# Performance work log

Measured on AMD Instinct MI355X. Metric: run time of the kernel, lower is better.

The kernel has to match this reference:

```python
import jax, jax.numpy as jnp
import numpy as np

NEG_SLOPE = 0.2  # PyG GATConv default leaky_relu slope
EPS = 1e-16      # PyG softmax denominator epsilon


def gat_conv(x, src, dst, n_nodes, W, att_src, att_dst, bias, concat):
    # x: [N, Din]; W: [Din, H*F]; att_src/att_dst: [H, F]; bias: [H*F] or [F]
    H, F = att_src.shape
    h = (x @ W).reshape(n_nodes, H, F)                 # [N, H, F]
    a_src = jnp.einsum('nhf,hf->nh', h, att_src)       # [N, H]
    a_dst = jnp.einsum('nhf,hf->nh', h, att_dst)       # [N, H]
    e = jax.nn.leaky_relu(a_src[src] + a_dst[dst], NEG_SLOPE)  # [E, H]
    # segment softmax over incoming edges of each destination node
    m = jax.ops.segment_max(e, dst, num_segments=n_nodes)      # [N, H]
    ex = jnp.exp(e - m[dst])                                   # [E, H]
    s = jax.ops.segment_sum(ex, dst, num_segments=n_nodes)     # [N, H]
    alpha = ex / (s[dst] + EPS)                                # [E, H]
    msg = alpha[:, :, None] * h[src]                           # [E, H, F]
    out = jax.ops.segment_sum(msg, dst, num_segments=n_nodes)  # [N, H, F]
    if concat:
        out = out.reshape(n_nodes, H * F)
    else:
        out = out.mean(axis=1)
    return out + bias


def setup_inputs() -> dict:
    key = jax.random.key(0)
    ks = jax.random.split(key, 12)
    N, E, Din, Fh, H, C = 50000, 800000, 512, 32, 8, 40
    x = jax.random.normal(ks[0], (N, Din), dtype=jnp.float32)
    edge_index = jax.random.randint(ks[1], (2, E), 0, N, dtype=jnp.int64)
    g1 = 1.0 / np.sqrt(Din)
    g2 = 1.0 / np.sqrt(H * Fh)
    return {
        'x': x,
        'edge_index': edge_index,
        'W1': jax.random.normal(ks[2], (Din, H * Fh), dtype=jnp.float32) * g1,
        'att_src1': jax.random.normal(ks[3], (H, Fh), dtype=jnp.float32) * g2,
        'att_dst1': jax.random.normal(ks[4], (H, Fh), dtype=jnp.float32) * g2,
        'b1': jnp.zeros((H * Fh,), dtype=jnp.float32),
        'W2': jax.random.normal(ks[5], (H * Fh, C), dtype=jnp.float32) * g2,
        'att_src2': jax.random.normal(ks[6], (1, C), dtype=jnp.float32) * 0.1,
        'att_dst2': jax.random.normal(ks[7], (1, C), dtype=jnp.float32) * 0.1,
        'b2': jnp.zeros((C,), dtype=jnp.float32),
    }


def reference(x, edge_index, W1, att_src1, att_dst1, b1, W2, att_src2, att_dst2, b2):
    N = x.shape[0]
    # PyG GATConv adds self-loops by default
    loop = jnp.arange(N, dtype=edge_index.dtype)
    src = jnp.concatenate([edge_index[0], loop])
    dst = jnp.concatenate([edge_index[1], loop])
    # eval mode: dropout layers are identity
    h = gat_conv(x, src, dst, N, W1, att_src1, att_dst1, b1, concat=True)
    h = jax.nn.elu(h)
    out = gat_conv(h, src, dst, N, W2, att_src2, att_dst2, b2, concat=False)
    return jax.nn.log_softmax(out, axis=1)
```

## Files before the change

### kernel.cpp

```cpp
#include <hip/hip_runtime.h>
#include <hip/hip_bf16.h>
#include <math.h>

#define NN_DIN 512
#define NN_HF  256
#define NN_H   8
#define NN_F   32
#define NN_C   40

typedef short bf16x8 __attribute__((ext_vector_type(8)));
typedef float f32x4 __attribute__((ext_vector_type(4)));

__device__ __forceinline__ unsigned short f2bf_rne(float x) {
    unsigned u = __builtin_bit_cast(unsigned, x);
    unsigned r = u + 0x7FFFu + ((u >> 16) & 1u);
    return (unsigned short)(r >> 16);
}
__device__ __forceinline__ float bfu2f(unsigned short s) {
    unsigned u = ((unsigned)s) << 16;
    return __builtin_bit_cast(float, u);
}

__global__ __launch_bounds__(256) void w1rne_kernel(
    const float* __restrict__ W1, unsigned short* __restrict__ Wh)
{
    __shared__ float tile[32][33];
    int bk = blockIdx.x * 32;
    int bn = blockIdx.y * 32;
    int tx = threadIdx.x & 31, ty = threadIdx.x >> 5;
    #pragma unroll
    for (int i = 0; i < 32; i += 8)
        tile[ty + i][tx] = W1[(size_t)(bk + ty + i) * NN_HF + bn + tx];
    __syncthreads();
    #pragma unroll
    for (int i = 0; i < 32; i += 8) {
        float v = tile[tx][ty + i];
        Wh[(size_t)(bn + ty + i) * NN_DIN + bk + tx] = f2bf_rne(v);
    }
}

#define G1_BM 64
#define G1_BN 256
#define G1_BK 64
#define G1_LDK 72

__global__ __launch_bounds__(256) void gemm1_kernel(
    const float* __restrict__ A, const unsigned short* __restrict__ BT,
    unsigned short* __restrict__ Cb, int M)
{
    __shared__ unsigned short Ah[G1_BM][G1_LDK];
    __shared__ unsigned short Bh[G1_BN][G1_LDK];
    const int m0 = blockIdx.x * G1_BM;
    const int tid = threadIdx.x;
    const int wave = tid >> 6, lane = tid & 63;
    const int wn = wave;
    const int lr = lane & 15, lg = lane >> 4;

    const int amr[4] = { (tid + 0*256) >> 4, (tid + 1*256) >> 4,
                         (tid + 2*256) >> 4, (tid + 3*256) >> 4 };
    const int akc = (tid & 15) << 2;
    const int bnr[8] = { (tid + 0*256) >> 3, (tid + 1*256) >> 3,
                         (tid + 2*256) >> 3, (tid + 3*256) >> 3,
                         (tid + 4*256) >> 3, (tid + 5*256) >> 3,
                         (tid + 6*256) >> 3, (tid + 7*256) >> 3 };
    const int bkc = (tid & 7) << 3;

    f32x4 acc[4][4];
    #pragma unroll
    for (int i = 0; i < 4; ++i)
        #pragma unroll
        for (int j = 0; j < 4; ++j) acc[i][j] = (f32x4){0.f, 0.f, 0.f, 0.f};

    float4 ra[4];
    bf16x8 rb[8];

    #pragma unroll
    for (int i = 0; i < 4; ++i) {
        ra[i] = make_float4(0.f, 0.f, 0.f, 0.f);
        if (m0 + amr[i] < M)
            ra[i] = *(const float4*)(A + (size_t)(m0 + amr[i]) * NN_DIN + akc);
    }
    #pragma unroll
    for (int i = 0; i < 8; ++i)
        rb[i] = *(const bf16x8*)(BT + (size_t)bnr[i] * NN_DIN + bkc);
    #pragma unroll
    for (int i = 0; i < 4; ++i) {
        ushort4 hv;
        hv.x = f2bf_rne(ra[i].x); hv.y = f2bf_rne(ra[i].y);
        hv.z = f2bf_rne(ra[i].z); hv.w = f2bf_rne(ra[i].w);
        *reinterpret_cast<ushort4*>(&Ah[amr[i]][akc]) = hv;
    }
    #pragma unroll
    for (int i = 0; i < 8; ++i)
        *reinterpret_cast<bf16x8*>(&Bh[bnr[i]][bkc]) = rb[i];
    __syncthreads();

    const int NSTEP = NN_DIN / G1_BK;
    for (int step = 0; step < NSTEP; ++step) {
        const bool last = (step == NSTEP - 1);
        if (!last) {
            int k0 = (step + 1) * G1_BK;
            #pragma unroll
            for (int i = 0; i < 4; ++i) {
                ra[i] = make_float4(0.f, 0.f, 0.f, 0.f);
                if (m0 + amr[i] < M)
                    ra[i] = *(const float4*)(A + (size_t)(m0 + amr[i]) * NN_DIN + k0 + akc);
            }
            #pragma unroll
            for (int i = 0; i < 8; ++i)
                rb[i] = *(const bf16x8*)(BT + (size_t)bnr[i] * NN_DIN + k0 + bkc);
        }
        #pragma unroll
        for (int ks = 0; ks < 2; ++ks) {
            const int kb = (ks << 5) + (lg << 3);
            bf16x8 fah[4], fbh[4];
            #pragma unroll
            for (int mi = 0; mi < 4; ++mi) {
                int m = (mi << 4) + lr;
                fah[mi] = *reinterpret_cast<const bf16x8*>(&Ah[m][kb]);
            }
            #pragma unroll
            for (int ni = 0; ni < 4; ++ni) {
                int n = (wn << 6) + (ni << 4) + lr;
                fbh[ni] = *reinterpret_cast<const bf16x8*>(&Bh[n][kb]);
            }
            #pragma unroll
            for (int mi = 0; mi < 4; ++mi)
                #pragma unroll
                for (int ni = 0; ni < 4; ++ni)
                    acc[mi][ni] = __builtin_amdgcn_mfma_f32_16x16x32_bf16(
                        fah[mi], fbh[ni], acc[mi][ni], 0, 0, 0);
        }
        __syncthreads();
        if (!last) {
            #pragma unroll
            for (int i = 0; i < 4; ++i) {
                ushort4 hv;
                hv.x = f2bf_rne(ra[i].x); hv.y = f2bf_rne(ra[i].y);
                hv.z = f2bf_rne(ra[i].z); hv.w = f2bf_rne(ra[i].w);
                *reinterpret_cast<ushort4*>(&Ah[amr[i]][akc]) = hv;
            }
            #pragma unroll
            for (int i = 0; i < 8; ++i)
                *reinterpret_cast<bf16x8*>(&Bh[bnr[i]][bkc]) = rb[i];
            __syncthreads();
        }
    }
    #pragma unroll
    for (int mi = 0; mi < 4; ++mi)
        #pragma unroll
        for (int ni = 0; ni < 4; ++ni)
            #pragma unroll
            for (int r = 0; r < 4; ++r) {
                int row = m0 + (mi << 4) + (lg << 2) + r;
                int col = (wn << 6) + (ni << 4) + lr;
                if (row < M)
                    Cb[(size_t)row * NN_HF + col] = f2bf_rne(acc[mi][ni][r]);
            }
}

__global__ __launch_bounds__(256) void attn1_kernel(
    const unsigned short* __restrict__ h1b, const float* __restrict__ att_s,
    const float* __restrict__ att_d, float* __restrict__ a1s,
    float* __restrict__ a1d)
{
    int n = blockIdx.x;
    int t = threadIdx.x;
    float hv = bfu2f(h1b[(size_t)n * NN_HF + t]);
    float ps = hv * att_s[t];
    float pd = hv * att_d[t];
    #pragma unroll
    for (int off = 16; off >= 1; off >>= 1) {
        ps += __shfl_down(ps, off, 32);
        pd += __shfl_down(pd, off, 32);
    }
    if ((t & 31) == 0) {
        a1s[n * NN_H + (t >> 5)] = ps;
        a1d[n * NN_H + (t >> 5)] = pd;
    }
}

__global__ void count_kernel(const int* __restrict__ dst, int* __restrict__ deg,
                             int E, int Nn)
{
    int e = blockIdx.x * blockDim.x + threadIdx.x;
    int Et = E + Nn;
    if (e >= Et) return;
    int d = (e < E) ? dst[e] : (e - E);
    atomicAdd(&deg[d], 1);
}

#define SCAN_CHUNK 1024
__global__ __launch_bounds__(256) void scan1_kernel(
    const int* __restrict__ deg, int* __restrict__ offs,
    int* __restrict__ bsums, int Nn)
{
    __shared__ int sh[256];
    int b = blockIdx.x, t = threadIdx.x;
    int base = b * SCAN_CHUNK + t * 4;
    int v[4];
    int tot = 0;
    #pragma unroll
    for (int i = 0; i < 4; ++i) {
        v[i] = (base + i < Nn) ? deg[base + i] : 0;
        tot += v[i];
    }
    sh[t] = tot;
    __syncthreads();
    for (int off = 1; off < 256; off <<= 1) {
        int y = (t >= off) ? sh[t - off] : 0;
        __syncthreads();
        sh[t] += y;
        __syncthreads();
    }
    int p = sh[t] - tot;
    #pragma unroll
    for (int i = 0; i < 4; ++i) {
        if (base + i < Nn) offs[base + i] = p;
        p += v[i];
    }
    if (t == 255) bsums[b] = sh[255];
}

__global__ void scan2_kernel(int* __restrict__ bsums, int nb)
{
    if (threadIdx.x == 0) {
        int run = 0;
        for (int i = 0; i < nb; ++i) {
            int tmp = bsums[i];
            bsums[i] = run;
            run += tmp;
        }
    }
}

__global__ void scan3_kernel(int* __restrict__ offs, const int* __restrict__ bsums,
                             int Nn, int Et)
{
    int i = blockIdx.x * blockDim.x + threadIdx.x;
    if (i < Nn) offs[i] += bsums[i >> 10];
    if (i == 0) offs[Nn] = Et;
}

__global__ void fill_kernel(const int* __restrict__ src, const int* __restrict__ dst,
                            const int* __restrict__ offs, int* __restrict__ cursor,
                            int* __restrict__ srcs, int E, int Nn)
{
    int e = blockIdx.x * blockDim.x + threadIdx.x;
    int Et = E + Nn;
    if (e >= Et) return;
    int d, s;
    if (e < E) { d = dst[e]; s = src[e]; }
    else       { d = e - E;  s = e - E;  }
    int pos = offs[d] + atomicAdd(&cursor[d], 1);
    srcs[pos] = s;
}

__global__ __launch_bounds__(256) void attw1_kernel(
    const float* __restrict__ a1s, const float* __restrict__ a1d,
    const int* __restrict__ offs, const int* __restrict__ srcs,
    float* __restrict__ alpha1, int Nn)
{
    int n = blockIdx.x * 4 + (threadIdx.x >> 6);
    if (n >= Nn) return;
    int lane = threadIdx.x & 63;
    int g = lane >> 3, h = lane & 7;
    int beg = offs[n], end = offs[n + 1];
    float adn = a1d[n * NN_H + h];
    float m = -3.0e38f, s = 0.f;
    for (int k = beg + g; k < end; k += 8) {
        int sN = srcs[k];
        float e = a1s[sN * NN_H + h] + adn;
        e = e > 0.f ? e : 0.2f * e;
        float nm = fmaxf(m, e);
        float sc = __expf(m - nm);
        s = s * sc + __expf(e - nm);
        m = nm;
    }
    #pragma unroll
    for (int off = 8; off < 64; off <<= 1) {
        float mo = __shfl_xor(m, off);
        float so = __shfl_xor(s, off);
        float nm = fmaxf(m, mo);
        s = s * __expf(m - nm) + so * __expf(mo - nm);
        m = nm;
    }
    float inv = 1.f / (s + 1e-16f);
    for (int k = beg + g; k < end; k += 8) {
        int sN = srcs[k];
        float e = a1s[sN * NN_H + h] + adn;
        e = e > 0.f ? e : 0.2f * e;
        alpha1[(size_t)k * NN_H + h] = __expf(e - m) * inv;
    }
}

__global__ __launch_bounds__(256) void agg1_kernel(
    const unsigned short* __restrict__ h1b, const float* __restrict__ alpha1,
    const int* __restrict__ offs, const int* __restrict__ srcs,
    const float* __restrict__ b1, unsigned short* __restrict__ hp1b, int Nn)
{
    int n = blockIdx.x * 4 + (threadIdx.x >> 6);
    if (n >= Nn) return;
    int lane = threadIdx.x & 63;
    int h = lane >> 3;
    int beg = offs[n], end = offs[n + 1];
    f32x4 a0 = {0.f,0.f,0.f,0.f}, a1 = a0, a2 = a0, a3 = a0;
    int k = beg;
    for (; k + 3 < end; k += 4) {
        int s0 = srcs[k], s1 = srcs[k+1], s2 = srcs[k+2], s3 = srcs[k+3];
        float w0 = alpha1[(size_t)k * NN_H + h];
        float w1 = alpha1[(size_t)(k+1) * NN_H + h];
        float w2 = alpha1[(size_t)(k+2) * NN_H + h];
        float w3 = alpha1[(size_t)(k+3) * NN_H + h];
        ushort4 v0 = *(const ushort4*)(h1b + (size_t)s0 * NN_HF + lane * 4);
        ushort4 v1 = *(const ushort4*)(h1b + (size_t)s1 * NN_HF + lane * 4);
        ushort4 v2 = *(const ushort4*)(h1b + (size_t)s2 * NN_HF + lane * 4);
        ushort4 v3 = *(const ushort4*)(h1b + (size_t)s3 * NN_HF + lane * 4);
        a0.x = fmaf(w0, bfu2f(v0.x), a0.x); a0.y = fmaf(w0, bfu2f(v0.y), a0.y);
        a0.z = fmaf(w0, bfu2f(v0.z), a0.z); a0.w = fmaf(w0, bfu2f(v0.w), a0.w);
        a1.x = fmaf(w1, bfu2f(v1.x), a1.x); a1.y = fmaf(w1, bfu2f(v1.y), a1.y);
        a1.z = fmaf(w1, bfu2f(v1.z), a1.z); a1.w = fmaf(w1, bfu2f(v1.w), a1.w);
        a2.x = fmaf(w2, bfu2f(v2.x), a2.x); a2.y = fmaf(w2, bfu2f(v2.y), a2.y);
        a2.z = fmaf(w2, bfu2f(v2.z), a2.z); a2.w = fmaf(w2, bfu2f(v2.w), a2.w);
        a3.x = fmaf(w3, bfu2f(v3.x), a3.x); a3.y = fmaf(w3, bfu2f(v3.y), a3.y);
        a3.z = fmaf(w3, bfu2f(v3.z), a3.z); a3.w = fmaf(w3, bfu2f(v3.w), a3.w);
    }
    for (; k < end; ++k) {
        int s0 = srcs[k];
        float w0 = alpha1[(size_t)k * NN_H + h];
        ushort4 v0 = *(const ushort4*)(h1b + (size_t)s0 * NN_HF + lane * 4);
        a0.x = fmaf(w0, bfu2f(v0.x), a0.x); a0.y = fmaf(w0, bfu2f(v0.y), a0.y);
        a0.z = fmaf(w0, bfu2f(v0.z), a0.z); a0.w = fmaf(w0, bfu2f(v0.w), a0.w);
    }
    f32x4 acc;
    acc[0] = (a0.x + a1.x) + (a2.x + a3.x);
    acc[1] = (a0.y + a1.y) + (a2.y + a3.y);
    acc[2] = (a0.z + a1.z) + (a2.z + a3.z);
    acc[3] = (a0.w + a1.w) + (a2.w + a3.w);
    float4 bb = *(const float4*)(b1 + lane * 4);
    float r0 = acc[0] + bb.x, r1 = acc[1] + bb.y;
    float r2 = acc[2] + bb.z, r3 = acc[3] + bb.w;
    r0 = r0 > 0.f ? r0 : __expf(r0) - 1.f;
    r1 = r1 > 0.f ? r1 : __expf(r1) - 1.f;
    r2 = r2 > 0.f ? r2 : __expf(r2) - 1.f;
    r3 = r3 > 0.f ? r3 : __expf(r3) - 1.f;
    ushort4 o = make_ushort4(f2bf_rne(r0), f2bf_rne(r1), f2bf_rne(r2), f2bf_rne(r3));
    *(ushort4*)(hp1b + (size_t)n * NN_HF + lane * 4) = o;
}

#define G2_ROWS 64
#define G2_KC   64

__global__ __launch_bounds__(256) void gemm2_kernel(
    const unsigned short* __restrict__ Ab, const float* __restrict__ W2,
    const float* __restrict__ att_s, const float* __restrict__ att_d,
    float* __restrict__ h2, float* __restrict__ a2s, float* __restrict__ a2d,
    int M)
{
    __shared__ float As[G2_ROWS][G2_KC + 1];
    __shared__ float Ws[G2_KC][NN_C];
    int m0 = blockIdx.x * G2_ROWS;
    int t = threadIdx.x;
    int rp = t >> 3;
    int cg = t & 7;
    int c0 = cg * 5;
    int r0 = rp * 2, r1 = r0 + 1;
    float acc[2][5] = {};
    for (int kc = 0; kc < NN_HF; kc += G2_KC) {
        #pragma unroll
        for (int i = 0; i < 4; ++i) {
            int g = t + i * 256;
            int r = g >> 4;
            int k4 = (g & 15) << 2;
            ushort4 v = make_ushort4(0, 0, 0, 0);
            if (m0 + r < M)
                v = *(const ushort4*)(Ab + (size_t)(m0 + r) * NN_HF + kc + k4);
            As[r][k4 + 0] = bfu2f(v.x); As[r][k4 + 1] = bfu2f(v.y);
            As[r][k4 + 2] = bfu2f(v.z); As[r][k4 + 3] = bfu2f(v.w);
        }
        #pragma unroll
        for (int i = 0; i < 10; ++i) {
            int g = t + i * 256;
            int k = g / NN_C, c = g % NN_C;
            Ws[k][c] = W2[(size_t)(kc + k) * NN_C + c];
        }
        __syncthreads();
        #pragma unroll 4
        for (int k = 0; k < G2_KC; ++k) {
            float a0 = As[r0][k];
            float a1 = As[r1][k];
            #pragma unroll
            for (int j = 0; j < 5; ++j) {
                float w = Ws[k][c0 + j];
                acc[0][j] += a0 * w;
                acc[1][j] += a1 * w;
            }
        }
        __syncthreads();
    }
    #pragma unroll
    for (int i = 0; i < 2; ++i) {
        int m = m0 + r0 + i;
        float ps = 0.f, pd = 0.f;
        #pragma unroll
        for (int j = 0; j < 5; ++j) {
            float v = acc[i][j];
            ps += v * att_s[c0 + j];
            pd += v * att_d[c0 + j];
            if (m < M) h2[(size_t)m * NN_C + c0 + j] = v;
        }
        #pragma unroll
        for (int off = 4; off >= 1; off >>= 1) {
            ps += __shfl_down(ps, off, 8);
            pd += __shfl_down(pd, off, 8);
        }
        if (cg == 0 && m < M) { a2s[m] = ps; a2d[m] = pd; }
    }
}

__global__ __launch_bounds__(256) void attw2_kernel(
    const float* __restrict__ a2s, const float* __restrict__ a2d,
    const int* __restrict__ offs, const int* __restrict__ srcs,
    float* __restrict__ alpha2, int Nn)
{
    int n = blockIdx.x * 4 + (threadIdx.x >> 6);
    if (n >= Nn) return;
    int lane = threadIdx.x & 63;
    int beg = offs[n], end = offs[n + 1];
    float adn = a2d[n];
    float m = -3.0e38f, s = 0.f;
    for (int k = beg + lane; k < end; k += 64) {
        int sN = srcs[k];
        float e = a2s[sN] + adn;
        e = e > 0.f ? e : 0.2f * e;
        float nm = fmaxf(m, e);
        float sc = __expf(m - nm);
        s = s * sc + __expf(e - nm);
        m = nm;
    }
    #pragma unroll
    for (int off = 1; off < 64; off <<= 1) {
        float mo = __shfl_xor(m, off);
        float so = __shfl_xor(s, off);
        float nm = fmaxf(m, mo);
        s = s * __expf(m - nm) + so * __expf(mo - nm);
        m = nm;
    }
    float inv = 1.f / (s + 1e-16f);
    for (int k = beg + lane; k < end; k += 64) {
        int sN = srcs[k];
        float e = a2s[sN] + adn;
        e = e > 0.f ? e : 0.2f * e;
        alpha2[k] = __expf(e - m) * inv;
    }
}

__global__ __launch_bounds__(256) void agg2_kernel(
    const float* __restrict__ h2, const float* __restrict__ alpha2,
    const int* __restrict__ offs, const int* __restrict__ srcs,
    const float* __restrict__ b2, float* __restrict__ out, int Nn)
{
    int n = blockIdx.x * 4 + (threadIdx.x >> 6);
    if (n >= Nn) return;
    int f = threadIdx.x & 63;
    int beg = offs[n], end = offs[n + 1];
    float a0 = 0.f, a1 = 0.f, a2 = 0.f, a3 = 0.f;
    int k = beg;
    for (; k + 3 < end; k += 4) {
        int s0 = srcs[k], s1 = srcs[k+1], s2 = srcs[k+2], s3 = srcs[k+3];
        float w0 = alpha2[k], w1 = alpha2[k+1], w2 = alpha2[k+2], w3 = alpha2[k+3];
        float h0 = (f < NN_C) ? h2[(size_t)s0 * NN_C + f] : 0.f;
        float h1 = (f < NN_C) ? h2[(size_t)s1 * NN_C + f] : 0.f;
        float h2v = (f < NN_C) ? h2[(size_t)s2 * NN_C + f] : 0.f;
        float h3 = (f < NN_C) ? h2[(size_t)s3 * NN_C + f] : 0.f;
        a0 = fmaf(w0, h0, a0); a1 = fmaf(w1, h1, a1);
        a2 = fmaf(w2, h2v, a2); a3 = fmaf(w3, h3, a3);
    }
    for (; k < end; ++k) {
        int s0 = srcs[k];
        float w0 = alpha2[k];
        float h0 = (f < NN_C) ? h2[(size_t)s0 * NN_C + f] : 0.f;
        a0 = fmaf(w0, h0, a0);
    }
    float acc = (a0 + a1) + (a2 + a3);
    float v = acc + ((f < NN_C) ? b2[f] : 0.f);
    float lg = (f < NN_C) ? v : -INFINITY;
    float mx = lg;
    #pragma unroll
    for (int off = 32; off >= 1; off >>= 1) mx = fmaxf(mx, __shfl_xor(mx, off));
    float w2e = (f < NN_C) ? __expf(lg - mx) : 0.f;
    float sum = w2e;
    #pragma unroll
    for (int off = 32; off >= 1; off >>= 1) sum += __shfl_xor(sum, off);
    if (f < NN_C) out[(size_t)n * NN_C + f] = lg - mx - __logf(sum);
}

extern "C" void kernel_launch(void* const* d_in, const int* in_sizes, int n_in,
                              void* d_out, int out_size, void* d_ws, size_t ws_size,
                              hipStream_t stream)
{
    const float* x    = (const float*)d_in[0];
    const int*   ei   = (const int*)d_in[1];
    const float* W1   = (const float*)d_in[2];
    const float* as1  = (const float*)d_in[3];
    const float* ad1  = (const float*)d_in[4];
    const float* b1   = (const float*)d_in[5];
    const float* W2   = (const float*)d_in[6];
    const float* as2  = (const float*)d_in[7];
    const float* ad2  = (const float*)d_in[8];
    const float* b2   = (const float*)d_in[9];
    float* out = (float*)d_out;

    int Nn = in_sizes[0] / NN_DIN;
    int E  = in_sizes[1] / 2;
    int Et = E + Nn;
    const int* srcIdx = ei;
    const int* dstIdx = ei + E;

    char* ws = (char*)d_ws;
    size_t off = 0;
    auto alloc = [&](size_t bytes) {
        void* p = ws + off;
        off = (off + bytes + 255) & ~(size_t)255;
        return p;
    };
    unsigned short* h1b  = (unsigned short*)alloc((size_t)Nn * NN_HF * 2);
    unsigned short* W1T  = (unsigned short*)alloc((size_t)NN_HF * NN_DIN * 2);
    unsigned short* hp1b = (unsigned short*)alloc((size_t)Nn * NN_HF * 2);
    float* a1s  = (float*)alloc((size_t)Nn * NN_H * 4);
    float* a1d  = (float*)alloc((size_t)Nn * NN_H * 4);
    float* h2   = (float*)alloc((size_t)Nn * NN_C * 4);
    float* a2s  = (float*)alloc((size_t)Nn * 4);
    float* a2d  = (float*)alloc((size_t)Nn * 4);
    float* alpha1 = (float*)alloc((size_t)Et * NN_H * 4);
    float* alpha2 = (float*)alloc((size_t)Et * 4);
    int*   deg  = (int*)alloc((size_t)Nn * 4);
    int*   offs = (int*)alloc((size_t)(Nn + 1) * 4);
    int*   bsums= (int*)alloc(1024 * 4);
    int*   curs = (int*)alloc((size_t)Nn * 4);
    int*   srcs = (int*)alloc((size_t)Et * 4);

    hipMemsetAsync(deg, 0, (size_t)Nn * 4, stream);
    hipMemsetAsync(curs, 0, (size_t)Nn * 4, stream);

    w1rne_kernel<<<dim3(NN_DIN / 32, NN_HF / 32), 256, 0, stream>>>(W1, W1T);

    gemm1_kernel<<<(Nn + G1_BM - 1) / G1_BM, 256, 0, stream>>>(x, W1T, h1b, Nn);

    attn1_kernel<<<Nn, 256, 0, stream>>>(h1b, as1, ad1, a1s, a1d);

    count_kernel<<<(Et + 255) / 256, 256, 0, stream>>>(dstIdx, deg, E, Nn);
    int nb = (Nn + SCAN_CHUNK - 1) / SCAN_CHUNK;
    scan1_kernel<<<nb, 256, 0, stream>>>(deg, offs, bsums, Nn);
    scan2_kernel<<<1, 64, 0, stream>>>(bsums, nb);
    scan3_kernel<<<(Nn + 255) / 256, 256, 0, stream>>>(offs, bsums, Nn, Et);
    fill_kernel<<<(Et + 255) / 256, 256, 0, stream>>>(srcIdx, dstIdx, offs, curs, srcs, E, Nn);

    attw1_kernel<<<(Nn + 3) / 4, 256, 0, stream>>>(a1s, a1d, offs, srcs, alpha1, Nn);
    agg1_kernel<<<(Nn + 3) / 4, 256, 0, stream>>>(h1b, alpha1, offs, srcs, b1, hp1b, Nn);

    gemm2_kernel<<<(Nn + G2_ROWS - 1) / G2_ROWS, 256, 0, stream>>>(
        hp1b, W2, as2, ad2, h2, a2s, a2d, Nn);

    attw2_kernel<<<(Nn + 3) / 4, 256, 0, stream>>>(a2s, a2d, offs, srcs, alpha2, Nn);
    agg2_kernel<<<(Nn + 3) / 4, 256, 0, stream>>>(h2, alpha2, offs, srcs, b2, out, Nn);
}
```

Measured before the change: 494.3 us.

## Fuse attention softmax into aggregation kernels and move gemm2 to bf16 MFMA

Merges attw1 into agg1 and attw2 into agg2. The softmax max and sum are now computed inside the aggregation kernel, and edge weights are recomputed on the fly instead of being written to and read back from alpha buffers. This removes two launches and the per-edge alpha traffic, at the cost of re-gathering a1s/a2s per edge. Separately, gemm2 is rewritten to use bf16 16x16x32 MFMA with a transposed, bf16-rounded W2 (padded to 48 columns) produced by a new small conversion kernel. The padding adds some wasted MFMA work, and W2 now passes through bf16 rounding.

```diff
diff --git a/kernel.cpp b/kernel.cpp
--- a/kernel.cpp
+++ b/kernel.cpp
@@ -37,6 +37,18 @@
         float v = tile[tx][ty + i];
         Wh[(size_t)(bn + ty + i) * NN_DIN + bk + tx] = f2bf_rne(v);
     }
+}
+
+__global__ __launch_bounds__(256) void w2rne_kernel(
+    const float* __restrict__ W2, unsigned short* __restrict__ W2T)
+{
+    int idx = blockIdx.x * 256 + threadIdx.x;
+    if (idx >= 48 * 256) return;
+    int c = idx >> 8;
+    int k = idx & 255;
+    unsigned short v = 0;
+    if (c < NN_C) v = f2bf_rne(W2[(size_t)k * NN_C + c]);
+    W2T[idx] = v;
 }
 
 #define G1_BM 64
@@ -256,25 +268,25 @@
     srcs[pos] = s;
 }
 
-__global__ __launch_bounds__(256) void attw1_kernel(
-    const float* __restrict__ a1s, const float* __restrict__ a1d,
-    const int* __restrict__ offs, const int* __restrict__ srcs,
-    float* __restrict__ alpha1, int Nn)
+__global__ __launch_bounds__(256) void agg1_kernel(
+    const unsigned short* __restrict__ h1b, const float* __restrict__ a1s,
+    const float* __restrict__ a1d, const int* __restrict__ offs,
+    const int* __restrict__ srcs, const float* __restrict__ b1,
+    unsigned short* __restrict__ hp1b, int Nn)
 {
     int n = blockIdx.x * 4 + (threadIdx.x >> 6);
     if (n >= Nn) return;
     int lane = threadIdx.x & 63;
-    int g = lane >> 3, h = lane & 7;
     int beg = offs[n], end = offs[n + 1];
-    float adn = a1d[n * NN_H + h];
+
+    int g = lane >> 3, hh = lane & 7;
+    float adn1 = a1d[n * NN_H + hh];
     float m = -3.0e38f, s = 0.f;
     for (int k = beg + g; k < end; k += 8) {
-        int sN = srcs[k];
-        float e = a1s[sN * NN_H + h] + adn;
+        float e = a1s[srcs[k] * NN_H + hh] + adn1;
         e = e > 0.f ? e : 0.2f * e;
         float nm = fmaxf(m, e);
-        float sc = __expf(m - nm);
-        s = s * sc + __expf(e - nm);
+        s = s * __expf(m - nm) + __expf(e - nm);
         m = nm;
     }
     #pragma unroll
@@ -286,32 +298,26 @@
         m = nm;
     }
     float inv = 1.f / (s + 1e-16f);
-    for (int k = beg + g; k < end; k += 8) {
-        int sN = srcs[k];
-        float e = a1s[sN * NN_H + h] + adn;
-        e = e > 0.f ? e : 0.2f * e;
-        alpha1[(size_t)k * NN_H + h] = __expf(e - m) * inv;
-    }
-}
-
-__global__ __launch_bounds__(256) void agg1_kernel(
-    const unsigned short* __restrict__ h1b, const float* __restrict__ alpha1,
-    const int* __restrict__ offs, const int* __restrict__ srcs,
-    const float* __restrict__ b1, unsigned short* __restrict__ hp1b, int Nn)
-{
-    int n = blockIdx.x * 4 + (threadIdx.x >> 6);
-    if (n >= Nn) return;
-    int lane = threadIdx.x & 63;
+
     int h = lane >> 3;
-    int beg = offs[n], end = offs[n + 1];
+    float mh   = __shfl(m, h);
+    float invh = __shfl(inv, h);
+    float adn  = __shfl(adn1, h);
+
     f32x4 a0 = {0.f,0.f,0.f,0.f}, a1 = a0, a2 = a0, a3 = a0;
     int k = beg;
     for (; k + 3 < end; k += 4) {
         int s0 = srcs[k], s1 = srcs[k+1], s2 = srcs[k+2], s3 = srcs[k+3];
-        float w0 = alpha1[(size_t)k * NN_H + h];
-        float w1 = alpha1[(size_t)(k+1) * NN_H + h];
-        float w2 = alpha1[(size_t)(k+2) * NN_H + h];
-        float w3 = alpha1[(size_t)(k+3) * NN_H + h];
+        float e0 = a1s[s0 * NN_H + h] + adn;
+        float e1 = a1s[s1 * NN_H + h] + adn;
+        float e2 = a1s[s2 * NN_H + h] + adn;
+        float e3 = a1s[s3 * NN_H + h] + adn;
+        e0 = e0 > 0.f ? e0 : 0.2f * e0;  e1 = e1 > 0.f ? e1 : 0.2f * e1;
+        e2 = e2 > 0.f ? e2 : 0.2f * e2;  e3 = e3 > 0.f ? e3 : 0.2f * e3;
+        float w0 = __expf(e0 - mh) * invh;
+        float w1 = __expf(e1 - mh) * invh;
+        float w2 = __expf(e2 - mh) * invh;
+        float w3 = __expf(e3 - mh) * invh;
         ushort4 v0 = *(const ushort4*)(h1b + (size_t)s0 * NN_HF + lane * 4);
         ushort4 v1 = *(const ushort4*)(h1b + (size_t)s1 * NN_HF + lane * 4);
         ushort4 v2 = *(const ushort4*)(h1b + (size_t)s2 * NN_HF + lane * 4);
@@ -327,7 +333,9 @@
     }
     for (; k < end; ++k) {
         int s0 = srcs[k];
-        float w0 = alpha1[(size_t)k * NN_H + h];
+        float e0 = a1s[s0 * NN_H + h] + adn;
+        e0 = e0 > 0.f ? e0 : 0.2f * e0;
+        float w0 = __expf(e0 - mh) * invh;
         ushort4 v0 = *(const ushort4*)(h1b + (size_t)s0 * NN_HF + lane * 4);
         a0.x = fmaf(w0, bfu2f(v0.x), a0.x); a0.y = fmaf(w0, bfu2f(v0.y), a0.y);
         a0.z = fmaf(w0, bfu2f(v0.z), a0.z); a0.w = fmaf(w0, bfu2f(v0.w), a0.w);
@@ -348,94 +356,132 @@
     *(ushort4*)(hp1b + (size_t)n * NN_HF + lane * 4) = o;
 }
 
-#define G2_ROWS 64
-#define G2_KC   64
+#define G2_BM 128
 
 __global__ __launch_bounds__(256) void gemm2_kernel(
-    const unsigned short* __restrict__ Ab, const float* __restrict__ W2,
+    const unsigned short* __restrict__ Ab, const unsigned short* __restrict__ W2T,
     const float* __restrict__ att_s, const float* __restrict__ att_d,
     float* __restrict__ h2, float* __restrict__ a2s, float* __restrict__ a2d,
     int M)
 {
-    __shared__ float As[G2_ROWS][G2_KC + 1];
-    __shared__ float Ws[G2_KC][NN_C];
-    int m0 = blockIdx.x * G2_ROWS;
-    int t = threadIdx.x;
-    int rp = t >> 3;
-    int cg = t & 7;
-    int c0 = cg * 5;
-    int r0 = rp * 2, r1 = r0 + 1;
-    float acc[2][5] = {};
-    for (int kc = 0; kc < NN_HF; kc += G2_KC) {
+    __shared__ unsigned short Ah[G2_BM][72];
+    __shared__ unsigned short Bh[48][72];
+    const int m0 = blockIdx.x * G2_BM;
+    const int tid = threadIdx.x;
+    const int wave = tid >> 6, lane = tid & 63;
+    const int lr = lane & 15, lg = lane >> 4;
+
+    f32x4 acc[2][3];
+    #pragma unroll
+    for (int i = 0; i < 2; ++i)
+        #pragma unroll
+        for (int j = 0; j < 3; ++j) acc[i][j] = (f32x4){0.f, 0.f, 0.f, 0.f};
+
+    for (int kc = 0; kc < NN_HF; kc += 64) {
         #pragma unroll
         for (int i = 0; i < 4; ++i) {
-            int g = t + i * 256;
-            int r = g >> 4;
-            int k4 = (g & 15) << 2;
-            ushort4 v = make_ushort4(0, 0, 0, 0);
+            int gi = tid + i * 256;
+            int r = gi >> 3;
+            int k8 = (gi & 7) << 3;
+            bf16x8 v = (bf16x8){0,0,0,0,0,0,0,0};
             if (m0 + r < M)
-                v = *(const ushort4*)(Ab + (size_t)(m0 + r) * NN_HF + kc + k4);
-            As[r][k4 + 0] = bfu2f(v.x); As[r][k4 + 1] = bfu2f(v.y);
-            As[r][k4 + 2] = bfu2f(v.z); As[r][k4 + 3] = bfu2f(v.w);
-        }
-        #pragma unroll
-        for (int i = 0; i < 10; ++i) {
-            int g = t + i * 256;
-            int k = g / NN_C, c = g % NN_C;
-            Ws[k][c] = W2[(size_t)(kc + k) * NN_C + c];
+                v = *(const bf16x8*)(Ab + (size_t)(m0 + r) * NN_HF + kc + k8);
+            *reinterpret_cast<bf16x8*>(&Ah[r][k8]) = v;
+        }
+        #pragma unroll
+        for (int i = 0; i < 2; ++i) {
+            int gi = tid + i * 256;
+            if (gi < 384) {
+                int r = gi >> 3;
+                int k8 = (gi & 7) << 3;
+                *reinterpret_cast<bf16x8*>(&Bh[r][k8]) =
+                    *(const bf16x8*)(W2T + (size_t)r * NN_HF + kc + k8);
+            }
         }
         __syncthreads();
-        #pragma unroll 4
-        for (int k = 0; k < G2_KC; ++k) {
-            float a0 = As[r0][k];
-            float a1 = As[r1][k];
-            #pragma unroll
-            for (int j = 0; j < 5; ++j) {
-                float w = Ws[k][c0 + j];
-                acc[0][j] += a0 * w;
-                acc[1][j] += a1 * w;
-            }
+        #pragma unroll
+        for (int ks = 0; ks < 2; ++ks) {
+            const int kb = (ks << 5) + (lg << 3);
+            bf16x8 fa[2], fb[3];
+            #pragma unroll
+            for (int mi = 0; mi < 2; ++mi) {
+                int r = (wave << 5) + (mi << 4) + lr;
+                fa[mi] = *reinterpret_cast<const bf16x8*>(&Ah[r][kb]);
+            }
+            #pragma unroll
+            for (int ni = 0; ni < 3; ++ni) {
+                int c = (ni << 4) + lr;
+                fb[ni] = *reinterpret_cast<const bf16x8*>(&Bh[c][kb]);
+            }
+            #pragma unroll
+            for (int mi = 0; mi < 2; ++mi)
+                #pragma unroll
+                for (int ni = 0; ni < 3; ++ni)
+                    acc[mi][ni] = __builtin_amdgcn_mfma_f32_16x16x32_bf16(
+                        fa[mi], fb[ni], acc[mi][ni], 0, 0, 0);
         }
         __syncthreads();
     }
-    #pragma unroll
-    for (int i = 0; i < 2; ++i) {
-        int m = m0 + r0 + i;
-        float ps = 0.f, pd = 0.f;
-        #pragma unroll
-        for (int j = 0; j < 5; ++j) {
-            float v = acc[i][j];
-            ps += v * att_s[c0 + j];
-            pd += v * att_d[c0 + j];
-            if (m < M) h2[(size_t)m * NN_C + c0 + j] = v;
-        }
-        #pragma unroll
-        for (int off = 4; off >= 1; off >>= 1) {
-            ps += __shfl_down(ps, off, 8);
-            pd += __shfl_down(pd, off, 8);
-        }
-        if (cg == 0 && m < M) { a2s[m] = ps; a2d[m] = pd; }
-    }
-}
-
-__global__ __launch_bounds__(256) void attw2_kernel(
-    const float* __restrict__ a2s, const float* __restrict__ a2d,
-    const int* __restrict__ offs, const int* __restrict__ srcs,
-    float* __restrict__ alpha2, int Nn)
+
+    float asv[3], adv[3];
+    #pragma unroll
+    for (int ni = 0; ni < 3; ++ni) {
+        int c = (ni << 4) + lr;
+        asv[ni] = (c < NN_C) ? att_s[c] : 0.f;
+        adv[ni] = (c < NN_C) ? att_d[c] : 0.f;
+    }
+    #pragma unroll
+    for (int mi = 0; mi < 2; ++mi) {
+        float ps[4] = {0.f,0.f,0.f,0.f}, pd[4] = {0.f,0.f,0.f,0.f};
+        #pragma unroll
+        for (int ni = 0; ni < 3; ++ni) {
+            int c = (ni << 4) + lr;
+            #pragma unroll
+            for (int r = 0; r < 4; ++r) {
+                float v = acc[mi][ni][r];
+                ps[r] = fmaf(v, asv[ni], ps[r]);
+                pd[r] = fmaf(v, adv[ni], pd[r]);
+                int row = m0 + (wave << 5) + (mi << 4) + (lg << 2) + r;
+                if (c < NN_C && row < M)
+                    h2[(size_t)row * NN_C + c] = v;
+            }
+        }
+        #pragma unroll
+        for (int off = 1; off < 16; off <<= 1) {
+            #pragma unroll
+            for (int r = 0; r < 4; ++r) {
+                ps[r] += __shfl_xor(ps[r], off);
+                pd[r] += __shfl_xor(pd[r], off);
+            }
+        }
+        if (lr == 0) {
+            #pragma unroll
+            for (int r = 0; r < 4; ++r) {
+                int row = m0 + (wave << 5) + (mi << 4) + (lg << 2) + r;
+                if (row < M) { a2s[row] = ps[r]; a2d[row] = pd[r]; }
+            }
+        }
+    }
+}
+
+__global__ __launch_bounds__(256) void agg2_kernel(
+    const float* __restrict__ h2, const float* __restrict__ a2s,
+    const float* __restrict__ a2d, const int* __restrict__ offs,
+    const int* __restrict__ srcs, const float* __restrict__ b2,
+    float* __restrict__ out, int Nn)
 {
     int n = blockIdx.x * 4 + (threadIdx.x >> 6);
     if (n >= Nn) return;
-    int lane = threadIdx.x & 63;
+    int f = threadIdx.x & 63;
     int beg = offs[n], end = offs[n + 1];
     float adn = a2d[n];
+
     float m = -3.0e38f, s = 0.f;
-    for (int k = beg + lane; k < end; k += 64) {
-        int sN = srcs[k];
-        float e = a2s[sN] + adn;
+    for (int k = beg + f; k < end; k += 64) {
+        float e = a2s[srcs[k]] + adn;
         e = e > 0.f ? e : 0.2f * e;
         float nm = fmaxf(m, e);
-        float sc = __expf(m - nm);
-        s = s * sc + __expf(e - nm);
+        s = s * __expf(m - nm) + __expf(e - nm);
         m = nm;
     }
     #pragma unroll
@@ -447,28 +493,17 @@
         m = nm;
     }
     float inv = 1.f / (s + 1e-16f);
-    for (int k = beg + lane; k < end; k += 64) {
-        int sN = srcs[k];
-        float e = a2s[sN] + adn;
-        e = e > 0.f ? e : 0.2f * e;
-        alpha2[k] = __expf(e - m) * inv;
-    }
-}
-
-__global__ __launch_bounds__(256) void agg2_kernel(
-    const float* __restrict__ h2, const float* __restrict__ alpha2,
-    const int* __restrict__ offs, const int* __restrict__ srcs,
-    const float* __restrict__ b2, float* __restrict__ out, int Nn)
-{
-    int n = blockIdx.x * 4 + (threadIdx.x >> 6);
-    if (n >= Nn) return;
-    int f = threadIdx.x & 63;
-    int beg = offs[n], end = offs[n + 1];
+
     float a0 = 0.f, a1 = 0.f, a2 = 0.f, a3 = 0.f;
     int k = beg;
     for (; k + 3 < end; k += 4) {
         int s0 = srcs[k], s1 = srcs[k+1], s2 = srcs[k+2], s3 = srcs[k+3];
-        float w0 = alpha2[k], w1 = alpha2[k+1], w2 = alpha2[k+2], w3 = alpha2[k+3];
+        float e0 = a2s[s0] + adn, e1 = a2s[s1] + adn;
+        float e2 = a2s[s2] + adn, e3 = a2s[s3] + adn;
+        e0 = e0 > 0.f ? e0 : 0.2f * e0;  e1 = e1 > 0.f ? e1 : 0.2f * e1;
+        e2 = e2 > 0.f ? e2 : 0.2f * e2;  e3 = e3 > 0.f ? e3 : 0.2f * e3;
+        float w0 = __expf(e0 - m) * inv, w1 = __expf(e1 - m) * inv;
+        float w2 = __expf(e2 - m) * inv, w3 = __expf(e3 - m) * inv;
         float h0 = (f < NN_C) ? h2[(size_t)s0 * NN_C + f] : 0.f;
         float h1 = (f < NN_C) ? h2[(size_t)s1 * NN_C + f] : 0.f;
         float h2v = (f < NN_C) ? h2[(size_t)s2 * NN_C + f] : 0.f;
@@ -478,7 +513,9 @@
     }
     for (; k < end; ++k) {
         int s0 = srcs[k];
-        float w0 = alpha2[k];
+        float e0 = a2s[s0] + adn;
+        e0 = e0 > 0.f ? e0 : 0.2f * e0;
+        float w0 = __expf(e0 - m) * inv;
         float h0 = (f < NN_C) ? h2[(size_t)s0 * NN_C + f] : 0.f;
         a0 = fmaf(w0, h0, a0);
     }
@@ -526,14 +563,13 @@
     };
     unsigned short* h1b  = (unsigned short*)alloc((size_t)Nn * NN_HF * 2);
     unsigned short* W1T  = (unsigned short*)alloc((size_t)NN_HF * NN_DIN * 2);
+    unsigned short* W2T  = (unsigned short*)alloc((size_t)48 * NN_HF * 2);
     unsigned short* hp1b = (unsigned short*)alloc((size_t)Nn * NN_HF * 2);
     float* a1s  = (float*)alloc((size_t)Nn * NN_H * 4);
     float* a1d  = (float*)alloc((size_t)Nn * NN_H * 4);
     float* h2   = (float*)alloc((size_t)Nn * NN_C * 4);
     float* a2s  = (float*)alloc((size_t)Nn * 4);
     float* a2d  = (float*)alloc((size_t)Nn * 4);
-    float* alpha1 = (float*)alloc((size_t)Et * NN_H * 4);
-    float* alpha2 = (float*)alloc((size_t)Et * 4);
     int*   deg  = (int*)alloc((size_t)Nn * 4);
     int*   offs = (int*)alloc((size_t)(Nn + 1) * 4);
     int*   bsums= (int*)alloc(1024 * 4);
@@ -544,6 +580,7 @@
     hipMemsetAsync(curs, 0, (size_t)Nn * 4, stream);
 
     w1rne_kernel<<<dim3(NN_DIN / 32, NN_HF / 32), 256, 0, stream>>>(W1, W1T);
+    w2rne_kernel<<<48, 256, 0, stream>>>(W2, W2T);
 
     gemm1_kernel<<<(Nn + G1_BM - 1) / G1_BM, 256, 0, stream>>>(x, W1T, h1b, Nn);
 
@@ -556,12 +593,10 @@
     scan3_kernel<<<(Nn + 255) / 256, 256, 0, stream>>>(offs, bsums, Nn, Et);
     fill_kernel<<<(Et + 255) / 256, 256, 0, stream>>>(srcIdx, dstIdx, offs, curs, srcs, E, Nn);
 
-    attw1_kernel<<<(Nn + 3) / 4, 256, 0, stream>>>(a1s, a1d, offs, srcs, alpha1, Nn);
-    agg1_kernel<<<(Nn + 3) / 4, 256, 0, stream>>>(h1b, alpha1, offs, srcs, b1, hp1b, Nn);
-
-    gemm2_kernel<<<(Nn + G2_ROWS - 1) / G2_ROWS, 256, 0, stream>>>(
-        hp1b, W2, as2, ad2, h2, a2s, a2d, Nn);
-
-    attw2_kernel<<<(Nn + 3) / 4, 256, 0, stream>>>(a2s, a2d, offs, srcs, alpha2, Nn);
-    agg2_kernel<<<(Nn + 3) / 4, 256, 0, stream>>>(h2, alpha2, offs, srcs, b2, out, Nn);
-}
+    agg1_kernel<<<(Nn + 3) / 4, 256, 0, stream>>>(h1b, a1s, a1d, offs, srcs, b1, hp1b, Nn);
+
+    gemm2_kernel<<<(Nn + G2_BM - 1) / G2_BM, 256, 0, stream>>>(
+        hp1b, W2T, as2, ad2, h2, a2s, a2d, Nn);
+
+    agg2_kernel<<<(Nn + 3) / 4, 256, 0, stream>>>(h2, a2s, a2d, offs, srcs, b2, out, Nn);
+}
```

After: 440.2 us. 1.12x faster.
